# Optimization experiments

Hardware: AMD Instinct MI355X
Metric: run time of the kernel (lower is better)

Reference implementation:

```python
import jax, jax.numpy as jnp
import numpy as np

# Standard asymmetric NF4 value table (bitsandbytes / flute nf_utils, bits=4, symmetric=False)
NF4_VALUES = np.array([
    -1.0, -0.6961928009986877, -0.5250730514526367, -0.39491748809814453,
    -0.28444138169288635, -0.18477343022823334, -0.09105003625154495, 0.0,
    0.07958029955625534, 0.16093020141124725, 0.2461123913526535,
    0.33791524171829224, 0.44070982933044434, 0.5626170039176941,
    0.7229568362236023, 1.0], dtype=np.float32)
# Pivots are midpoints between consecutive values -> nearest-value bucketing via searchsorted
NF4_PIVOTS = (NF4_VALUES[:-1] + NF4_VALUES[1:]) / 2.0

GROUP_SIZE = 64
IN_FEATURES = 4096
OUT_FEATURES = 4096
BATCH, SEQ = 4, 2048


def setup_inputs() -> dict:
    key = jax.random.key(0)
    k1, k2 = jax.random.split(key)
    inp = jax.random.normal(k1, (BATCH, SEQ, IN_FEATURES), dtype=jnp.float32)
    weight = jax.random.normal(k2, (OUT_FEATURES, IN_FEATURES), dtype=jnp.float32) * 0.02
    # scales initialized exactly as in __init__: per-group absmax of the weight
    scales = jnp.max(jnp.abs(weight.reshape(-1, GROUP_SIZE)), axis=1, keepdims=True)  # [out*in/64, 1]
    return {
        "inp": inp,
        "weight": weight,
        "scales": scales,
        "values": jnp.asarray(NF4_VALUES),
        "pivots": jnp.asarray(NF4_PIVOTS),
    }


def _manual_nf4(weight, scales, values, pivots, group_size):
    # groupwise absmax-normalize, nearest-value lookup via pivot search, dequantize
    w = weight.reshape(-1, group_size)                 # [n_groups, group_size]
    scaled = jnp.clip(w / scales, -1.0, 1.0)
    idx = jnp.searchsorted(pivots, scaled)             # nearest NF4 code
    qweight = values[idx] * scales                     # dequantized bf16-style weight
    return qweight.reshape(weight.shape)


def reference(inp, weight, scales, values, pivots):
    qweight = _manual_nf4(weight, scales, values, pivots, GROUP_SIZE)  # [out, in]
    # F.linear(inp, qweight), bias=None
    return jnp.einsum('bsi,oi->bso', inp, qweight)
```

## Files before the change

### kernel.cpp

```cpp
#include <hip/hip_runtime.h>
#include <hip/hip_bf16.h>
#include <stdint.h>

#define M_DIM 8192
#define N_DIM 4096
#define K_DIM 4096
#define BM 256
#define BN 256
#define BK 64
#define NT (K_DIM / BK)

#define CVT_BLOCKS 8192
#define DQ_BLOCKS  8192

typedef float f32x16 __attribute__((ext_vector_type(16)));
typedef __bf16 bf16x8 __attribute__((ext_vector_type(8)));
typedef short s16x8 __attribute__((ext_vector_type(8)));

template <typename AB>
__device__ __forceinline__ auto mfma_32x32x16(AB a, AB b, f32x16 c, int)
    -> decltype(__builtin_amdgcn_mfma_f32_32x32x16_bf16(a, b, c, 0, 0, 0)) {
  return __builtin_amdgcn_mfma_f32_32x32x16_bf16(a, b, c, 0, 0, 0);
}
template <typename AB>
__device__ __forceinline__ f32x16 mfma_32x32x16(AB a, AB b, f32x16 c, long) {
  return __builtin_amdgcn_mfma_f32_32x32x16_bf16(
      __builtin_bit_cast(s16x8, a), __builtin_bit_cast(s16x8, b), c, 0, 0, 0);
}

__device__ __forceinline__ uint16_t f2b(float f) {
  union { float f; uint32_t u; } v; v.f = f;
  uint32_t u = v.u;
  u += 0x7FFFu + ((u >> 16) & 1u);
  return (uint16_t)(u >> 16);
}

__global__ __launch_bounds__(256) void prep(const float* __restrict__ inp,
                                            uint16_t* __restrict__ A_bf16,
                                            const float* __restrict__ w,
                                            const float* __restrict__ scales,
                                            const float* __restrict__ values,
                                            const float* __restrict__ pivots,
                                            uint16_t* __restrict__ B_bf16) {
  if (blockIdx.x < CVT_BLOCKS) {
    size_t t0 = (size_t)blockIdx.x * 256 + threadIdx.x;
    const float4* pin = (const float4*)inp;
    uint2* pout = (uint2*)A_bf16;
#pragma unroll
    for (int it = 0; it < 4; ++it) {
      size_t i = t0 + (size_t)it * ((size_t)CVT_BLOCKS * 256);
      float4 a = pin[i];
      uint2 o;
      o.x = (uint32_t)f2b(a.x) | ((uint32_t)f2b(a.y) << 16);
      o.y = (uint32_t)f2b(a.z) | ((uint32_t)f2b(a.w) << 16);
      pout[i] = o;
    }
  } else {
    __shared__ float sv[16];
    if (threadIdx.x < 16) sv[threadIdx.x] = values[threadIdx.x];
    float pv[15];
#pragma unroll
    for (int j = 0; j < 15; ++j) pv[j] = pivots[j];
    __syncthreads();
    size_t t0 = (size_t)(blockIdx.x - CVT_BLOCKS) * 256 + threadIdx.x;
    const float4* pw = (const float4*)w;
    uint2* pout = (uint2*)B_bf16;
#pragma unroll
    for (int it = 0; it < 2; ++it) {
      size_t i = t0 + (size_t)it * ((size_t)DQ_BLOCKS * 256);
      float scale = scales[i >> 4];
      float psc[15];
#pragma unroll
      for (int j = 0; j < 15; ++j) psc[j] = pv[j] * scale;
      float4 a = pw[i];
      float e[4] = {a.x, a.y, a.z, a.w};
      uint32_t hw[4];
#pragma unroll
      for (int k = 0; k < 4; ++k) {
        int idx = 0;
#pragma unroll
        for (int j = 0; j < 15; ++j) idx += (psc[j] < e[k]) ? 1 : 0;
        hw[k] = f2b(sv[idx] * scale);
      }
      uint2 o = {hw[0] | (hw[1] << 16), hw[2] | (hw[3] << 16)};
      pout[i] = o;
    }
  }
}


#define GLL(SRC, LOFF)                                                        \
  __builtin_amdgcn_global_load_lds(                                           \
      (__attribute__((address_space(1))) void*)(void*)(SRC),                  \
      (__attribute__((address_space(3))) void*)(smem + (LOFF)), 16, 0, 0)

#define STAGE_A(NB, KH, KEL)                                                  \
  do {                                                                        \
    GLL(Ab + gs0 + (KEL) + (KH) * 32, (NB) * 32768u + (KH) * 16384u + l0);    \
    GLL(Ab + gs1 + (KEL) + (KH) * 32, (NB) * 32768u + (KH) * 16384u + l1);    \
  } while (0)
#define STAGE_B(NB, KH, KEL)                                                  \
  do {                                                                        \
    GLL(Bb + gs0 + (KEL) + (KH) * 32,                                         \
        65536u + (NB) * 32768u + (KH) * 16384u + l0);                         \
    GLL(Bb + gs1 + (KEL) + (KH) * 32,                                         \
        65536u + (NB) * 32768u + (KH) * 16384u + l1);                         \
  } while (0)

#define SYNC4()                                                               \
  do {                                                                        \
    asm volatile("s_waitcnt vmcnt(4)" ::: "memory");                          \
    __builtin_amdgcn_s_barrier();                                             \
    __builtin_amdgcn_sched_barrier(0);                                        \
  } while (0)

#define READ6(A0, A1, A2, A3, B0, B1, CUR, KH, CB)                            \
  do {                                                                        \
    const uint32_t _ab = (CUR) * 32768u + (KH) * 16384u + aoff;               \
    const uint32_t _bb = 65536u + (CUR) * 32768u + (KH) * 16384u + boff;      \
    A0 = *(const bf16x8*)(smem + _ab + (CB));                                 \
    A1 = *(const bf16x8*)(smem + _ab + 2048u + (CB));                         \
    A2 = *(const bf16x8*)(smem + _ab + 4096u + (CB));                         \
    A3 = *(const bf16x8*)(smem + _ab + 6144u + (CB));                         \
    B0 = *(const bf16x8*)(smem + _bb + (CB));                                 \
    B1 = *(const bf16x8*)(smem + _bb + 2048u + (CB));                         \
  } while (0)

#define MFMA8(A0, A1, A2, A3, B0, B1)                                         \
  do {                                                                        \
    acc[0][0] = mfma_32x32x16(A0, B0, acc[0][0], 0);                          \
    acc[0][1] = mfma_32x32x16(A0, B1, acc[0][1], 0);                          \
    acc[1][0] = mfma_32x32x16(A1, B0, acc[1][0], 0);                          \
    acc[1][1] = mfma_32x32x16(A1, B1, acc[1][1], 0);                          \
    acc[2][0] = mfma_32x32x16(A2, B0, acc[2][0], 0);                          \
    acc[2][1] = mfma_32x32x16(A2, B1, acc[2][1], 0);                          \
    acc[3][0] = mfma_32x32x16(A3, B0, acc[3][0], 0);                          \
    acc[3][1] = mfma_32x32x16(A3, B1, acc[3][1], 0);                          \
  } while (0)

#define HALF(CUR, NB, KH, KEL)                                                \
  do {                                                                        \
    bf16x8 xa0, xa1, xa2, xa3, xb0, xb1;                                      \
    bf16x8 ya0, ya1, ya2, ya3, yb0, yb1;                                      \
    READ6(xa0, xa1, xa2, xa3, xb0, xb1, CUR, KH, cb0);                        \
    READ6(ya0, ya1, ya2, ya3, yb0, yb1, CUR, KH, cb1);                        \
    STAGE_A(NB, KH, KEL);                                                     \
    asm volatile("s_waitcnt lgkmcnt(6)" ::: "memory");                        \
    __builtin_amdgcn_sched_barrier(0);                                        \
    __builtin_amdgcn_s_setprio(1);                                            \
    MFMA8(xa0, xa1, xa2, xa3, xb0, xb1);                                      \
    __builtin_amdgcn_s_setprio(0);                                            \
    STAGE_B(NB, KH, KEL);                                                     \
    asm volatile("s_waitcnt lgkmcnt(0)" ::: "memory");                        \
    __builtin_amdgcn_sched_barrier(0);                                        \
    __builtin_amdgcn_s_setprio(1);                                            \
    MFMA8(ya0, ya1, ya2, ya3, yb0, yb1);                                      \
    __builtin_amdgcn_s_setprio(0);                                            \
  } while (0)

#define TILE(CUR, NB, KEL)                                                    \
  do {                                                                        \
    HALF(CUR, NB, 0u, KEL);                                                   \
    SYNC4();                                                                  \
    HALF(CUR, NB, 1u, KEL);                                                   \
    SYNC4();                                                                  \
  } while (0)

__global__ __launch_bounds__(512, 2) void gemm_bt(const uint16_t* __restrict__ A,
                                                  const uint16_t* __restrict__ B,
                                                  float* __restrict__ C) {
  __shared__ char smem[131072];
  const int tid = threadIdx.x;
  const int wave = tid >> 6;
  const int lane = tid & 63;

  const int bid = blockIdx.x;
  const int wg = (bid & 7) * 64 + (bid >> 3);
  const int bm = wg >> 4;
  const int bn = wg & 15;

  const int wm = wave >> 2;
  const int wn = wave & 3;
  const int r31 = lane & 31;
  const int hi = lane >> 5;

  const int swz = (r31 >> 1) & 3;
  const uint32_t cb0 = (uint32_t)(((hi ^ swz) * 16));
  const uint32_t cb1 = (uint32_t)((((2 + hi) ^ swz) * 16));
  const uint32_t aoff = (uint32_t)(wm * 8192 + r31 * 64);
  const uint32_t boff = (uint32_t)(wn * 4096 + r31 * 64);

  const int s0 = wave * 128 + lane;
  const int r0 = s0 >> 2;
  const uint32_t gs0 =
      (uint32_t)r0 * K_DIM + (uint32_t)((((s0 & 3) ^ ((r0 >> 1) & 3)) * 8));
  const int s1 = s0 + 64;
  const int r1 = s1 >> 2;
  const uint32_t gs1 =
      (uint32_t)r1 * K_DIM + (uint32_t)((((s1 & 3) ^ ((r1 >> 1) & 3)) * 8));
  const uint32_t l0 = (uint32_t)(wave * 2048);
  const uint32_t l1 = l0 + 1024u;

  const uint16_t* Ab = A + (size_t)bm * BM * K_DIM;
  const uint16_t* Bb = B + (size_t)bn * BN * K_DIM;

  f32x16 acc[4][2] = {};

  STAGE_A(0u, 0u, 0u);
  STAGE_B(0u, 0u, 0u);
  STAGE_A(0u, 1u, 0u);
  STAGE_B(0u, 1u, 0u);
  asm volatile("s_waitcnt vmcnt(4)" ::: "memory");
  __builtin_amdgcn_s_barrier();
  __builtin_amdgcn_sched_barrier(0);

  for (int kt2 = 0; kt2 < NT; kt2 += 2) {
    const uint32_t kel0 = (uint32_t)(kt2 + 1) * BK;
    const uint32_t kel1 =
        (uint32_t)((kt2 + 2 < NT) ? (kt2 + 2) : (NT - 1)) * BK;
    TILE(0u, 1u, kel0);
    TILE(1u, 0u, kel1);
  }

  asm volatile("s_waitcnt vmcnt(0)" ::: "memory");

  const int crow0 = bm * BM + wm * 128;
  const int ccol0 = bn * BN + wn * 64 + r31;
#pragma unroll
  for (int i = 0; i < 4; ++i)
#pragma unroll
    for (int j = 0; j < 2; ++j)
#pragma unroll
      for (int reg = 0; reg < 16; ++reg) {
        int row = i * 32 + (reg & 3) + 8 * (reg >> 2) + 4 * hi;
        C[(size_t)(crow0 + row) * N_DIM + ccol0 + j * 32] = acc[i][j][reg];
      }
}

extern "C" void kernel_launch(void* const* d_in, const int* in_sizes, int n_in,
                              void* d_out, int out_size, void* d_ws, size_t ws_size,
                              hipStream_t stream) {
  const float* inp    = (const float*)d_in[0];
  const float* weight = (const float*)d_in[1];
  const float* scales = (const float*)d_in[2];
  const float* values = (const float*)d_in[3];
  const float* pivots = (const float*)d_in[4];
  float* out = (float*)d_out;

  uint16_t* A_bf16 = (uint16_t*)d_ws;
  uint16_t* B_bf16 = A_bf16 + (size_t)M_DIM * K_DIM;

  prep<<<CVT_BLOCKS + DQ_BLOCKS, 256, 0, stream>>>(inp, A_bf16, weight, scales, values,
                                                   pivots, B_bf16);
  gemm_bt<<<dim3(512), 512, 0, stream>>>(A_bf16, B_bf16, out);
}
```

Measured before the change: 520.5 us.

## Restructure GEMM main loop to one barrier per tile with interleaved LDS reads

The GEMM inner tile now issues all global-to-LDS prefetches for the next tile early. It interleaves LDS fragment reads with MFMA groups under lgkmcnt waits and synchronises once per BK tile instead of twice. The LDS swizzle adds an extra XOR bit from row bit 3 to reduce bank conflicts on fragment reads, applied consistently on store and load. The dequant half of the prep kernel uses half as many blocks with four iterations each. The single end-of-tile vmcnt(0) wait may expose more memory latency than the previous vmcnt(4) scheme.

```diff
diff --git a/kernel.cpp b/kernel.cpp
--- a/kernel.cpp
+++ b/kernel.cpp
@@ -11,7 +11,7 @@
 #define NT (K_DIM / BK)
 
 #define CVT_BLOCKS 8192
-#define DQ_BLOCKS  8192
+#define DQ_BLOCKS  4096
 
 typedef float f32x16 __attribute__((ext_vector_type(16)));
 typedef __bf16 bf16x8 __attribute__((ext_vector_type(8)));
@@ -66,7 +66,7 @@
     const float4* pw = (const float4*)w;
     uint2* pout = (uint2*)B_bf16;
 #pragma unroll
-    for (int it = 0; it < 2; ++it) {
+    for (int it = 0; it < 4; ++it) {
       size_t i = t0 + (size_t)it * ((size_t)DQ_BLOCKS * 256);
       float scale = scales[i >> 4];
       float psc[15];
@@ -107,10 +107,14 @@
         65536u + (NB) * 32768u + (KH) * 16384u + l1);                         \
   } while (0)
 
-#define SYNC4()                                                               \
-  do {                                                                        \
-    asm volatile("s_waitcnt vmcnt(4)" ::: "memory");                          \
-    __builtin_amdgcn_s_barrier();                                             \
+#define LGKM6                                                                 \
+  do {                                                                        \
+    asm volatile("s_waitcnt lgkmcnt(6)" ::: "memory");                        \
+    __builtin_amdgcn_sched_barrier(0);                                        \
+  } while (0)
+#define LGKM0                                                                 \
+  do {                                                                        \
+    asm volatile("s_waitcnt lgkmcnt(0)" ::: "memory");                        \
     __builtin_amdgcn_sched_barrier(0);                                        \
   } while (0)
 
@@ -119,15 +123,16 @@
     const uint32_t _ab = (CUR) * 32768u + (KH) * 16384u + aoff;               \
     const uint32_t _bb = 65536u + (CUR) * 32768u + (KH) * 16384u + boff;      \
     A0 = *(const bf16x8*)(smem + _ab + (CB));                                 \
+    B0 = *(const bf16x8*)(smem + _bb + (CB));                                 \
+    B1 = *(const bf16x8*)(smem + _bb + 2048u + (CB));                         \
     A1 = *(const bf16x8*)(smem + _ab + 2048u + (CB));                         \
     A2 = *(const bf16x8*)(smem + _ab + 4096u + (CB));                         \
     A3 = *(const bf16x8*)(smem + _ab + 6144u + (CB));                         \
-    B0 = *(const bf16x8*)(smem + _bb + (CB));                                 \
-    B1 = *(const bf16x8*)(smem + _bb + 2048u + (CB));                         \
-  } while (0)
-
-#define MFMA8(A0, A1, A2, A3, B0, B1)                                         \
-  do {                                                                        \
+  } while (0)
+
+#define MM8(A0, A1, A2, A3, B0, B1)                                           \
+  do {                                                                        \
+    __builtin_amdgcn_s_setprio(1);                                            \
     acc[0][0] = mfma_32x32x16(A0, B0, acc[0][0], 0);                          \
     acc[0][1] = mfma_32x32x16(A0, B1, acc[0][1], 0);                          \
     acc[1][0] = mfma_32x32x16(A1, B0, acc[1][0], 0);                          \
@@ -136,34 +141,33 @@
     acc[2][1] = mfma_32x32x16(A2, B1, acc[2][1], 0);                          \
     acc[3][0] = mfma_32x32x16(A3, B0, acc[3][0], 0);                          \
     acc[3][1] = mfma_32x32x16(A3, B1, acc[3][1], 0);                          \
-  } while (0)
-
-#define HALF(CUR, NB, KH, KEL)                                                \
+    __builtin_amdgcn_sched_barrier(0);                                        \
+    __builtin_amdgcn_s_setprio(0);                                            \
+  } while (0)
+
+#define TILE(CUR, NB, KEL)                                                    \
   do {                                                                        \
     bf16x8 xa0, xa1, xa2, xa3, xb0, xb1;                                      \
     bf16x8 ya0, ya1, ya2, ya3, yb0, yb1;                                      \
-    READ6(xa0, xa1, xa2, xa3, xb0, xb1, CUR, KH, cb0);                        \
-    READ6(ya0, ya1, ya2, ya3, yb0, yb1, CUR, KH, cb1);                        \
-    STAGE_A(NB, KH, KEL);                                                     \
-    asm volatile("s_waitcnt lgkmcnt(6)" ::: "memory");                        \
-    __builtin_amdgcn_sched_barrier(0);                                        \
-    __builtin_amdgcn_s_setprio(1);                                            \
-    MFMA8(xa0, xa1, xa2, xa3, xb0, xb1);                                      \
-    __builtin_amdgcn_s_setprio(0);                                            \
-    STAGE_B(NB, KH, KEL);                                                     \
-    asm volatile("s_waitcnt lgkmcnt(0)" ::: "memory");                        \
-    __builtin_amdgcn_sched_barrier(0);                                        \
-    __builtin_amdgcn_s_setprio(1);                                            \
-    MFMA8(ya0, ya1, ya2, ya3, yb0, yb1);                                      \
-    __builtin_amdgcn_s_setprio(0);                                            \
-  } while (0)
-
-#define TILE(CUR, NB, KEL)                                                    \
-  do {                                                                        \
-    HALF(CUR, NB, 0u, KEL);                                                   \
-    SYNC4();                                                                  \
-    HALF(CUR, NB, 1u, KEL);                                                   \
-    SYNC4();                                                                  \
+    READ6(xa0, xa1, xa2, xa3, xb0, xb1, CUR, 0u, cb0);            \
+    STAGE_A(NB, 0u, KEL);                                                     \
+    STAGE_B(NB, 0u, KEL);                                                     \
+    READ6(ya0, ya1, ya2, ya3, yb0, yb1, CUR, 0u, cb1);            \
+    LGKM6;                                                 \
+    MM8(xa0, xa1, xa2, xa3, xb0, xb1);                                        \
+    READ6(xa0, xa1, xa2, xa3, xb0, xb1, CUR, 1u, cb0);            \
+    STAGE_A(NB, 1u, KEL);                                                     \
+    STAGE_B(NB, 1u, KEL);                                                     \
+    LGKM6;                                                 \
+    MM8(ya0, ya1, ya2, ya3, yb0, yb1);                                        \
+    READ6(ya0, ya1, ya2, ya3, yb0, yb1, CUR, 1u, cb1);            \
+    LGKM6;                                                 \
+    MM8(xa0, xa1, xa2, xa3, xb0, xb1);                                        \
+    LGKM0;                                                 \
+    MM8(ya0, ya1, ya2, ya3, yb0, yb1);                                        \
+    asm volatile("s_waitcnt vmcnt(0)" ::: "memory");  \
+    __builtin_amdgcn_s_barrier();                                             \
+    __builtin_amdgcn_sched_barrier(0);                                        \
   } while (0)
 
 __global__ __launch_bounds__(512, 2) void gemm_bt(const uint16_t* __restrict__ A,
@@ -184,7 +188,7 @@
   const int r31 = lane & 31;
   const int hi = lane >> 5;
 
-  const int swz = (r31 >> 1) & 3;
+  const int swz = ((r31 >> 1) & 3) ^ ((r31 >> 3) & 1);
   const uint32_t cb0 = (uint32_t)(((hi ^ swz) * 16));
   const uint32_t cb1 = (uint32_t)((((2 + hi) ^ swz) * 16));
   const uint32_t aoff = (uint32_t)(wm * 8192 + r31 * 64);
@@ -193,11 +197,13 @@
   const int s0 = wave * 128 + lane;
   const int r0 = s0 >> 2;
   const uint32_t gs0 =
-      (uint32_t)r0 * K_DIM + (uint32_t)((((s0 & 3) ^ ((r0 >> 1) & 3)) * 8));
+      (uint32_t)r0 * K_DIM +
+      (uint32_t)((((s0 & 3) ^ (((r0 >> 1) & 3) ^ ((r0 >> 3) & 1))) * 8));
   const int s1 = s0 + 64;
   const int r1 = s1 >> 2;
   const uint32_t gs1 =
-      (uint32_t)r1 * K_DIM + (uint32_t)((((s1 & 3) ^ ((r1 >> 1) & 3)) * 8));
+      (uint32_t)r1 * K_DIM +
+      (uint32_t)((((s1 & 3) ^ (((r1 >> 1) & 3) ^ ((r1 >> 3) & 1))) * 8));
   const uint32_t l0 = (uint32_t)(wave * 2048);
   const uint32_t l1 = l0 + 1024u;
 
@@ -210,19 +216,17 @@
   STAGE_B(0u, 0u, 0u);
   STAGE_A(0u, 1u, 0u);
   STAGE_B(0u, 1u, 0u);
-  asm volatile("s_waitcnt vmcnt(4)" ::: "memory");
+  asm volatile("s_waitcnt vmcnt(0)" ::: "memory");
   __builtin_amdgcn_s_barrier();
   __builtin_amdgcn_sched_barrier(0);
 
-  for (int kt2 = 0; kt2 < NT; kt2 += 2) {
-    const uint32_t kel0 = (uint32_t)(kt2 + 1) * BK;
+  for (int kt = 0; kt < NT; kt += 2) {
+    const uint32_t kel0 = (uint32_t)(kt + 1) * BK;
     const uint32_t kel1 =
-        (uint32_t)((kt2 + 2 < NT) ? (kt2 + 2) : (NT - 1)) * BK;
+        (uint32_t)((kt + 2 < NT) ? (kt + 2) : (NT - 1)) * BK;
     TILE(0u, 1u, kel0);
     TILE(1u, 0u, kel1);
   }
-
-  asm volatile("s_waitcnt vmcnt(0)" ::: "memory");
 
   const int crow0 = bm * BM + wm * 128;
   const int ccol0 = bn * BN + wn * 64 + r31;
@@ -250,7 +254,7 @@
   uint16_t* A_bf16 = (uint16_t*)d_ws;
   uint16_t* B_bf16 = A_bf16 + (size_t)M_DIM * K_DIM;
 
-  prep<<<CVT_BLOCKS + DQ_BLOCKS, 256, 0, stream>>>(inp, A_bf16, weight, scales, values,
-                                                   pivots, B_bf16);
+  prep<<<CVT_BLOCKS + DQ_BLOCKS, 256, 0, stream>>>(inp, A_bf16, weight, scales,
+                                                   values, pivots, B_bf16);
   gemm_bt<<<dim3(512), 512, 0, stream>>>(A_bf16, B_bf16, out);
 }
```

Result: slower. 541.0 us (+3.9%).
